# Kernel tuning notes

Measured on AMD Instinct MI355X. Metric: run time of the kernel, lower is better.

Reference implementation:

```python
import jax, jax.numpy as jnp
import numpy as np

N_NODES = 100_000
N_EDGES = 1_600_000
N_GRAPHS = 512
NODE_TYPE_BUCKETS = 256
IDENT_BUCKETS = 50_000
NODE_EMB = 64
IDENT_EMB = 32
IN_DIM = NODE_EMB + IDENT_EMB + 6  # 102
HID = 128
NUM_CATS = 10


def setup_inputs() -> dict:
    key = jax.random.key(0)
    ks = jax.random.split(key, 24)
    p = lambda k, shp: (jax.random.normal(k, shp, dtype=jnp.float32) * 0.05)
    return {
        "node_type_ids": jax.random.randint(ks[0], (N_NODES,), 0, NODE_TYPE_BUCKETS + 2),
        "ident_hash_ids": jax.random.randint(ks[1], (N_NODES,), 0, IDENT_BUCKETS + 2),
        "literal_flags": jax.random.uniform(ks[2], (N_NODES, 5), dtype=jnp.float32),
        "node_depth": jax.random.randint(ks[3], (N_NODES,), 0, 60),
        "edge_index": jax.random.randint(ks[4], (2, N_EDGES), 0, N_NODES),
        "batch_index": jnp.sort(jax.random.randint(ks[5], (N_NODES,), 0, N_GRAPHS)),
        "emb_node": p(ks[6], (NODE_TYPE_BUCKETS + 2, NODE_EMB)),
        "emb_ident": p(ks[7], (IDENT_BUCKETS + 2, IDENT_EMB)),
        "W_self0": p(ks[8], (IN_DIM, HID)), "b_self0": p(ks[9], (HID,)),
        "W_neigh0": p(ks[10], (IN_DIM, HID)), "b_neigh0": p(ks[11], (HID,)),
        "W_self1": p(ks[12], (HID, HID)), "b_self1": p(ks[13], (HID,)),
        "W_neigh1": p(ks[14], (HID, HID)), "b_neigh1": p(ks[15], (HID,)),
        "W_risk": p(ks[16], (HID, 1)), "b_risk": p(ks[17], (1,)),
        "W_cat": p(ks[18], (HID, NUM_CATS)), "b_cat": p(ks[19], (NUM_CATS,)),
    }


def reference(node_type_ids, ident_hash_ids, literal_flags, node_depth,
              edge_index, batch_index, emb_node, emb_ident,
              W_self0, b_self0, W_neigh0, b_neigh0,
              W_self1, b_self1, W_neigh1, b_neigh1,
              W_risk, b_risk, W_cat, b_cat):
    n = node_type_ids.shape[0]
    # node features: [N, 64+32+5+1]
    depth = node_depth.astype(jnp.float32)[:, None]
    depth = depth / jnp.maximum(depth.max(), 1.0)
    x = jnp.concatenate([emb_node[node_type_ids], emb_ident[ident_hash_ids],
                         literal_flags, depth], axis=-1)
    src, dst = edge_index[0], edge_index[1]
    # in-degree, shared across layers (clamped to 1)
    deg = jax.ops.segment_sum(jnp.ones_like(dst, jnp.float32), dst, num_segments=n)
    inv_deg = (1.0 / jnp.maximum(deg, 1.0))[:, None]

    def sage(x, Ws, bs, Wn, bn):
        agg = jax.ops.segment_sum(x[src], dst, num_segments=n)  # gather+scatter-sum
        neigh = agg * inv_deg
        return jax.nn.relu(x @ Ws + bs + neigh @ Wn + bn)

    x = sage(x, W_self0, b_self0, W_neigh0, b_neigh0)
    x = sage(x, W_self1, b_self1, W_neigh1, b_neigh1)

    # global mean pool over graphs
    pooled = jax.ops.segment_sum(x, batch_index, num_segments=N_GRAPHS)
    counts = jax.ops.segment_sum(jnp.ones((n,), jnp.float32), batch_index,
                                 num_segments=N_GRAPHS)
    g = pooled / jnp.maximum(counts, 1.0)[:, None]

    risk_logit = (g @ W_risk + b_risk)[:, 0]
    category_logits = g @ W_cat + b_cat
    return risk_logit, category_logits
```

## Files before the change

kernel.cpp:

```cpp
#include <hip/hip_runtime.h>
#include <cstdint>
#include <cstddef>

#define HIDDIM 128
#define NGRAPH_MAX 512
#define LDSPAD 136
#define NBKT_MAX 512

using short8 = __attribute__((ext_vector_type(8))) short;
using f32x4  = __attribute__((ext_vector_type(4))) float;

__device__ __forceinline__ unsigned short f2bf(float x) {
    union { float f; uint32_t u; } v; v.f = x;
    uint32_t r = v.u + 0x7fffu + ((v.u >> 16) & 1u);
    return (unsigned short)(r >> 16);
}
__device__ __forceinline__ uint32_t pack2(float a, float b) {
    return (uint32_t)f2bf(a) | ((uint32_t)f2bf(b) << 16);
}
__device__ __forceinline__ float bflo(uint32_t u) { return __uint_as_float(u << 16); }
__device__ __forceinline__ float bfhi(uint32_t u) { return __uint_as_float(u & 0xffff0000u); }

__global__ void k_prep(const int* __restrict__ nt, const int* __restrict__ ih,
                       const float* __restrict__ flags, const int* __restrict__ depth,
                       const float* __restrict__ embN, const float* __restrict__ embI,
                       const int* __restrict__ edst, const int* __restrict__ batch,
                       const float* __restrict__ Wn0, const float* __restrict__ Ws0,
                       const float* __restrict__ Wn1, const float* __restrict__ Ws1,
                       int K0, int N, int E, int G,
                       unsigned short* __restrict__ x0, unsigned short* __restrict__ Wt,
                       int* __restrict__ bcount, int* __restrict__ counts,
                       int* __restrict__ maxd,
                       int nbF, int nbC, int nbN) {
    __shared__ int hist[NBKT_MAX];
    __shared__ int red[256];
    int b = blockIdx.x, t = threadIdx.x;
    if (b < nbF) {
        int idx = b * 256 + t;
        int i = idx >> 4;
        int seg = idx & 15;
        if (i >= N) return;
        uint4 o = make_uint4(0u, 0u, 0u, 0u);
        if (seg < 8) {
            const float4* r = (const float4*)(embN + (size_t)nt[i] * 64 + seg * 8);
            float4 v0 = r[0], v1 = r[1];
            o.x = pack2(v0.x, v0.y); o.y = pack2(v0.z, v0.w);
            o.z = pack2(v1.x, v1.y); o.w = pack2(v1.z, v1.w);
        } else if (seg < 12) {
            const float4* r = (const float4*)(embI + (size_t)ih[i] * 32 + (seg - 8) * 8);
            float4 v0 = r[0], v1 = r[1];
            o.x = pack2(v0.x, v0.y); o.y = pack2(v0.z, v0.w);
            o.z = pack2(v1.x, v1.y); o.w = pack2(v1.z, v1.w);
        } else if (seg == 12) {
            const float* fp = flags + (size_t)i * 5;
            o.x = pack2(fp[0], fp[1]);
            o.y = pack2(fp[2], fp[3]);
            o.z = pack2(fp[4], 0.f);
        }
        *(uint4*)(x0 + (size_t)i * HIDDIM + seg * 8) = o;
    } else if (b < nbF + nbC) {
        hist[t] = 0; hist[t + 256] = 0;
        __syncthreads();
        int c0 = (b - nbF) * 4096;
        int ce = min(4096, E - c0);
        for (int i = t; i < ce; i += 256)
            atomicAdd(&hist[edst[c0 + i] >> 8], 1);
        __syncthreads();
        for (int bb = t; bb < NBKT_MAX; bb += 256)
            if (hist[bb]) atomicAdd(&bcount[bb], hist[bb]);
    } else if (b < nbF + nbC + nbN) {
        for (int g = t; g < G; g += 256) hist[g] = 0;
        __syncthreads();
        int i = (b - nbF - nbC) * 256 + t;
        int d = 0;
        if (i < N) {
            atomicAdd(&hist[batch[i]], 1);
            d = depth[i];
        }
        red[t] = d;
        __syncthreads();
        for (int off = 128; off > 0; off >>= 1) {
            if (t < off) red[t] = max(red[t], red[t + off]);
            __syncthreads();
        }
        if (t == 0) atomicMax(maxd, red[0]);
        for (int g = t; g < G; g += 256)
            if (hist[g]) atomicAdd(&counts[g], hist[g]);
    } else {
        int idx = (b - nbF - nbC - nbN) * 256 + t;
        int mat = idx >> 14;
        int rem = idx & 16383;
        int n = rem >> 7, k = rem & 127;
        const float* W = (mat == 0) ? Wn0 : (mat == 1) ? Ws0 : (mat == 2) ? Wn1 : Ws1;
        int K = (mat < 2) ? K0 : HIDDIM;
        Wt[(size_t)mat * HIDDIM * HIDDIM + n * HIDDIM + k] =
            (k < K) ? f2bf(W[(size_t)k * HIDDIM + n]) : (unsigned short)0;
    }
}

__global__ void k_scan2x(const int* __restrict__ bcount, int* __restrict__ boff,
                         int* __restrict__ bcur, int* __restrict__ rowptr,
                         const int* __restrict__ counts, int* __restrict__ gstart,
                         const int* __restrict__ depth, const int* __restrict__ maxd,
                         unsigned short* __restrict__ x0,
                         int nbkt, int N, int E, int G) {
    __shared__ int sd[512];
    int b = blockIdx.x, t = threadIdx.x;
    if (b == 0) {
        int v = (t < nbkt) ? bcount[t] : 0;
        sd[t] = v;
        __syncthreads();
        for (int off = 1; off < 512; off <<= 1) {
            int x = (t >= off) ? sd[t - off] : 0;
            __syncthreads();
            sd[t] += x;
            __syncthreads();
        }
        if (t < nbkt) { boff[t] = sd[t] - v; bcur[t] = sd[t] - v; }
        if (t == 0) { boff[nbkt] = E; rowptr[N] = E; }
    } else if (b == 1) {
        int v = (t < G) ? counts[t] : 0;
        sd[t] = v;
        __syncthreads();
        for (int off = 1; off < 512; off <<= 1) {
            int x = (t >= off) ? sd[t - off] : 0;
            __syncthreads();
            sd[t] += x;
            __syncthreads();
        }
        if (t < G) gstart[t] = sd[t] - v;
        if (t == G - 1) gstart[G] = sd[t];
    } else {
        int i = (b - 2) * 512 + t;
        if (i < N) {
            float md = fmaxf((float)(*maxd), 1.0f);
            x0[(size_t)i * HIDDIM + 101] = f2bf((float)depth[i] / md);
        }
    }
}

__global__ void k_bscatter(const int* __restrict__ src, const int* __restrict__ dst,
                           int* __restrict__ bcur, int2* __restrict__ ebuf, int E, int nbkt) {
    __shared__ int2 stage[4096];
    __shared__ int hist[NBKT_MAX];
    __shared__ int ofs[NBKT_MAX];
    __shared__ int cur[NBKT_MAX];
    __shared__ int gbase[NBKT_MAX];
    __shared__ int scanbuf[256];
    int t = threadIdx.x;
    int c0 = blockIdx.x * 4096;
    int ce = min(4096, E - c0);

    hist[t] = 0; hist[t + 256] = 0;
    __syncthreads();
    for (int i = t; i < ce; i += 256)
        atomicAdd(&hist[dst[c0 + i] >> 8], 1);
    __syncthreads();
    int h2a = hist[2 * t], h2b = hist[2 * t + 1];
    int ps = h2a + h2b;
    scanbuf[t] = ps;
    __syncthreads();
    for (int off = 1; off < 256; off <<= 1) {
        int x = (t >= off) ? scanbuf[t - off] : 0;
        __syncthreads();
        scanbuf[t] += x;
        __syncthreads();
    }
    int ex = scanbuf[t] - ps;
    ofs[2 * t] = ex;           cur[2 * t] = ex;
    ofs[2 * t + 1] = ex + h2a; cur[2 * t + 1] = ex + h2a;
    __syncthreads();
    for (int i = t; i < ce; i += 256) {
        int d = dst[c0 + i];
        int p = atomicAdd(&cur[d >> 8], 1);
        stage[p] = make_int2(src[c0 + i], d);
    }
    __syncthreads();
    for (int b = t; b < nbkt; b += 256) {
        int c = hist[b];
        gbase[b] = c ? atomicAdd(&bcur[b], c) : 0;
    }
    __syncthreads();
    for (int j = t; j < ce; j += 256) {
        int2 p = stage[j];
        int b = p.y >> 8;
        ebuf[gbase[b] + (j - ofs[b])] = p;
    }
}

__global__ void k_build(const int2* __restrict__ ebuf, const int* __restrict__ boff,
                        int* __restrict__ rowptr, float* __restrict__ invd,
                        int* __restrict__ srcs, int N) {
    __shared__ int ldeg[256];
    __shared__ int lofs[256];
    __shared__ int lcur[256];
    int b = blockIdx.x, t = threadIdx.x;
    int n0 = b << 8;
    int s = boff[b], e = boff[b + 1];
    ldeg[t] = 0;
    __syncthreads();
    for (int i = s + t; i < e; i += 256)
        atomicAdd(&ldeg[ebuf[i].y & 255], 1);
    __syncthreads();
    int v = ldeg[t];
    lofs[t] = v;
    __syncthreads();
    for (int off = 1; off < 256; off <<= 1) {
        int x = (t >= off) ? lofs[t - off] : 0;
        __syncthreads();
        lofs[t] += x;
        __syncthreads();
    }
    int excl = lofs[t] - v;
    int node = n0 + t;
    if (node < N) {
        rowptr[node] = s + excl;
        invd[node] = 1.0f / (float)max(v, 1);
    }
    lcur[t] = excl;
    __syncthreads();
    for (int i = s + t; i < e; i += 256) {
        int2 p = ebuf[i];
        int slot = atomicAdd(&lcur[p.y & 255], 1);
        srcs[s + slot] = p.x;
    }
}

__global__ __launch_bounds__(256, 2) void k_gemm2(
    const unsigned short* __restrict__ X,
    const unsigned short* __restrict__ Wtn, const unsigned short* __restrict__ Wts,
    int N, const float* __restrict__ bias_s, const float* __restrict__ bias_n,
    unsigned short* __restrict__ Y, unsigned short* __restrict__ S) {
    __shared__ unsigned short Bn[128 * LDSPAD];
    __shared__ unsigned short Bs[128 * LDSPAD];
    int t = threadIdx.x;
    int rowBase = blockIdx.x << 7;

    #pragma unroll
    for (int it = 0; it < 8; it++) {
        int idx = t + it * 256;
        int n = idx >> 4, seg = idx & 15;
        *(uint4*)&Bn[n * LDSPAD + seg * 8] = *(const uint4*)(Wtn + n * HIDDIM + seg * 8);
        *(uint4*)&Bs[n * LDSPAD + seg * 8] = *(const uint4*)(Wts + n * HIDDIM + seg * 8);
    }

    int lane = t & 63;
    int wv = t >> 6;
    int ml = lane & 15;
    int quad = lane >> 4;
    int m0 = wv * 32;

    const uint4* X4 = (const uint4*)X;
    int gr0 = rowBase + m0 + ml;
    int gr1 = gr0 + 16;
    uint4 af0[4], af1[4];
    #pragma unroll
    for (int kt = 0; kt < 4; kt++) {
        uint4 z = make_uint4(0u, 0u, 0u, 0u);
        af0[kt] = (gr0 < N) ? X4[(size_t)gr0 * 16 + kt * 4 + quad] : z;
        af1[kt] = (gr1 < N) ? X4[(size_t)gr1 * 16 + kt * 4 + quad] : z;
    }
    __syncthreads();

    f32x4 accY[2][8], accS[2][8];
    #pragma unroll
    for (int i = 0; i < 2; i++)
        #pragma unroll
        for (int j = 0; j < 8; j++) {
            accY[i][j] = (f32x4){0.f, 0.f, 0.f, 0.f};
            accS[i][j] = (f32x4){0.f, 0.f, 0.f, 0.f};
        }

    #pragma unroll
    for (int kt = 0; kt < 4; kt++) {
        int ko = kt * 32 + quad * 8;
        short8 a0 = *(short8*)&af0[kt];
        short8 a1 = *(short8*)&af1[kt];
        #pragma unroll
        for (int nt = 0; nt < 8; nt++) {
            short8 bn = *(const short8*)&Bn[(nt * 16 + ml) * LDSPAD + ko];
            accY[0][nt] = __builtin_amdgcn_mfma_f32_16x16x32_bf16(a0, bn, accY[0][nt], 0, 0, 0);
            accY[1][nt] = __builtin_amdgcn_mfma_f32_16x16x32_bf16(a1, bn, accY[1][nt], 0, 0, 0);
            short8 bs = *(const short8*)&Bs[(nt * 16 + ml) * LDSPAD + ko];
            accS[0][nt] = __builtin_amdgcn_mfma_f32_16x16x32_bf16(a0, bs, accS[0][nt], 0, 0, 0);
            accS[1][nt] = __builtin_amdgcn_mfma_f32_16x16x32_bf16(a1, bs, accS[1][nt], 0, 0, 0);
        }
    }

    float bsum[8];
    #pragma unroll
    for (int nt = 0; nt < 8; nt++) {
        int col = nt * 16 + ml;
        bsum[nt] = bias_s[col] + bias_n[col];
    }

    __syncthreads();
    #pragma unroll
    for (int mt = 0; mt < 2; mt++) {
        int lrow0 = m0 + mt * 16 + quad * 4;
        #pragma unroll
        for (int r = 0; r < 4; r++)
            #pragma unroll
            for (int nt = 0; nt < 8; nt++) {
                Bn[(lrow0 + r) * LDSPAD + nt * 16 + ml] = f2bf(accY[mt][nt][r]);
                Bs[(lrow0 + r) * LDSPAD + nt * 16 + ml] = f2bf(accS[mt][nt][r] + bsum[nt]);
            }
    }
    __syncthreads();
    #pragma unroll
    for (int it = 0; it < 8; it++) {
        int idx = t + it * 256;
        int r = idx >> 4, seg = idx & 15;
        int gr = rowBase + r;
        if (gr < N) {
            *(uint4*)(Y + (size_t)gr * HIDDIM + seg * 8) = *(const uint4*)&Bn[r * LDSPAD + seg * 8];
            *(uint4*)(S + (size_t)gr * HIDDIM + seg * 8) = *(const uint4*)&Bs[r * LDSPAD + seg * 8];
        }
    }
}

__global__ void k_aggc(const uint4* __restrict__ y4, const uint4* __restrict__ s4,
                       const int* __restrict__ rp, const int* __restrict__ srcs,
                       const float* __restrict__ invd, uint4* __restrict__ xo, int N) {
    int t = threadIdx.x;
    int lane = t & 63;
    int q = lane >> 4;
    int cl = lane & 15;
    int d = blockIdx.x * 4 + (t >> 6);
    if (d >= N) return;
    int s = rp[d], e = rp[d + 1];
    float a0 = 0.f, a1 = 0.f, a2 = 0.f, a3 = 0.f,
          a4 = 0.f, a5 = 0.f, a6 = 0.f, a7 = 0.f;
#define ACC8(u) { a0 += bflo(u.x); a1 += bfhi(u.x); a2 += bflo(u.y); a3 += bfhi(u.y); \
                  a4 += bflo(u.z); a5 += bfhi(u.z); a6 += bflo(u.w); a7 += bfhi(u.w); }
    for (int base = s; base < e; base += 64) {
        int m = min(64, e - base);
        int idx = (lane < m) ? srcs[base + lane] : 0;
        int j = 0;
        for (; j + 16 <= m; j += 16) {
            int i0 = __shfl(idx, j + q, 64);
            int i1 = __shfl(idx, j + 4 + q, 64);
            int i2 = __shfl(idx, j + 8 + q, 64);
            int i3 = __shfl(idx, j + 12 + q, 64);
            uint4 u0 = y4[(size_t)i0 * 16 + cl];
            uint4 u1 = y4[(size_t)i1 * 16 + cl];
            uint4 u2 = y4[(size_t)i2 * 16 + cl];
            uint4 u3 = y4[(size_t)i3 * 16 + cl];
            ACC8(u0); ACC8(u1); ACC8(u2); ACC8(u3);
        }
        for (; j + 4 <= m; j += 4) {
            int id = __shfl(idx, j + q, 64);
            uint4 u = y4[(size_t)id * 16 + cl];
            ACC8(u);
        }
        if (j < m) {
            int id = __shfl(idx, min(j + q, m - 1), 64);
            if (q < m - j) {
                uint4 u = y4[(size_t)id * 16 + cl];
                ACC8(u);
            }
        }
    }
#undef ACC8
    a0 += __shfl_down(a0, 32, 64); a1 += __shfl_down(a1, 32, 64);
    a2 += __shfl_down(a2, 32, 64); a3 += __shfl_down(a3, 32, 64);
    a4 += __shfl_down(a4, 32, 64); a5 += __shfl_down(a5, 32, 64);
    a6 += __shfl_down(a6, 32, 64); a7 += __shfl_down(a7, 32, 64);
    a0 += __shfl_down(a0, 16, 64); a1 += __shfl_down(a1, 16, 64);
    a2 += __shfl_down(a2, 16, 64); a3 += __shfl_down(a3, 16, 64);
    a4 += __shfl_down(a4, 16, 64); a5 += __shfl_down(a5, 16, 64);
    a6 += __shfl_down(a6, 16, 64); a7 += __shfl_down(a7, 16, 64);
    if (q == 0) {
        float iv = invd[d];
        uint4 su = s4[(size_t)d * 16 + cl];
        uint4 o;
        o.x = pack2(fmaxf(bflo(su.x) + a0 * iv, 0.f), fmaxf(bfhi(su.x) + a1 * iv, 0.f));
        o.y = pack2(fmaxf(bflo(su.y) + a2 * iv, 0.f), fmaxf(bfhi(su.y) + a3 * iv, 0.f));
        o.z = pack2(fmaxf(bflo(su.z) + a4 * iv, 0.f), fmaxf(bfhi(su.z) + a5 * iv, 0.f));
        o.w = pack2(fmaxf(bflo(su.w) + a6 * iv, 0.f), fmaxf(bfhi(su.w) + a7 * iv, 0.f));
        xo[(size_t)d * 16 + cl] = o;
    }
}

__global__ void k_poolhead(const uint32_t* __restrict__ x, const int* __restrict__ gstart,
                           const int* __restrict__ counts,
                           const float* __restrict__ Wr, const float* __restrict__ br,
                           const float* __restrict__ Wc, const float* __restrict__ bc,
                           float* __restrict__ out, int G) {
    __shared__ float red[3][128];
    __shared__ float rowf[128];
    int gr = blockIdx.x, t = threadIdx.x;
    int wv = t >> 6, lane = t & 63;
    int half = lane >> 5, cl = lane & 31;
    int s = gstart[gr], e = gstart[gr + 1];
    const uint2* x2 = (const uint2*)x;
    float a0 = 0.f, a1 = 0.f, a2 = 0.f, a3 = 0.f;
    for (int r0 = s + wv * 2 + half; r0 < e; r0 += 32) {
        uint2 u0 = x2[(size_t)r0 * 32 + cl];
        int r1 = r0 + 8, r2 = r0 + 16, r3 = r0 + 24;
        uint2 u1 = make_uint2(0u, 0u), u2 = make_uint2(0u, 0u), u3 = make_uint2(0u, 0u);
        if (r1 < e) u1 = x2[(size_t)r1 * 32 + cl];
        if (r2 < e) u2 = x2[(size_t)r2 * 32 + cl];
        if (r3 < e) u3 = x2[(size_t)r3 * 32 + cl];
        a0 += bflo(u0.x); a1 += bfhi(u0.x); a2 += bflo(u0.y); a3 += bfhi(u0.y);
        a0 += bflo(u1.x); a1 += bfhi(u1.x); a2 += bflo(u1.y); a3 += bfhi(u1.y);
        a0 += bflo(u2.x); a1 += bfhi(u2.x); a2 += bflo(u2.y); a3 += bfhi(u2.y);
        a0 += bflo(u3.x); a1 += bfhi(u3.x); a2 += bflo(u3.y); a3 += bfhi(u3.y);
    }
    a0 += __shfl_down(a0, 32, 64);
    a1 += __shfl_down(a1, 32, 64);
    a2 += __shfl_down(a2, 32, 64);
    a3 += __shfl_down(a3, 32, 64);
    if (half == 0 && wv > 0) {
        red[wv - 1][cl * 4 + 0] = a0;
        red[wv - 1][cl * 4 + 1] = a1;
        red[wv - 1][cl * 4 + 2] = a2;
        red[wv - 1][cl * 4 + 3] = a3;
    }
    __syncthreads();
    if (wv == 0 && half == 0) {
        a0 += red[0][cl * 4 + 0] + red[1][cl * 4 + 0] + red[2][cl * 4 + 0];
        a1 += red[0][cl * 4 + 1] + red[1][cl * 4 + 1] + red[2][cl * 4 + 1];
        a2 += red[0][cl * 4 + 2] + red[1][cl * 4 + 2] + red[2][cl * 4 + 2];
        a3 += red[0][cl * 4 + 3] + red[1][cl * 4 + 3] + red[2][cl * 4 + 3];
        float inv = 1.0f / fmaxf((float)counts[gr], 1.0f);
        rowf[cl * 4 + 0] = a0 * inv;
        rowf[cl * 4 + 1] = a1 * inv;
        rowf[cl * 4 + 2] = a2 * inv;
        rowf[cl * 4 + 3] = a3 * inv;
    }
    __syncthreads();
    if (t == 0) {
        float s2 = 0.f;
        for (int k = 0; k < 128; k++) s2 += rowf[k] * Wr[k];
        out[gr] = s2 + br[0];
    } else if (t <= 10) {
        int j = t - 1;
        float s2 = 0.f;
        for (int k = 0; k < 128; k++) s2 += rowf[k] * Wc[k * 10 + j];
        out[G + gr * 10 + j] = s2 + bc[j];
    }
}

extern "C" void kernel_launch(void* const* d_in, const int* in_sizes, int n_in,
                              void* d_out, int out_size, void* d_ws, size_t ws_size,
                              hipStream_t stream) {
    const int*   nt    = (const int*)d_in[0];
    const int*   ih    = (const int*)d_in[1];
    const float* flags = (const float*)d_in[2];
    const int*   depth = (const int*)d_in[3];
    const int*   eidx  = (const int*)d_in[4];
    const int*   batch = (const int*)d_in[5];
    const float* embN  = (const float*)d_in[6];
    const float* embI  = (const float*)d_in[7];
    const float* Ws0   = (const float*)d_in[8];
    const float* bs0   = (const float*)d_in[9];
    const float* Wn0   = (const float*)d_in[10];
    const float* bn0   = (const float*)d_in[11];
    const float* Ws1   = (const float*)d_in[12];
    const float* bs1   = (const float*)d_in[13];
    const float* Wn1   = (const float*)d_in[14];
    const float* bn1   = (const float*)d_in[15];
    const float* Wr    = (const float*)d_in[16];
    const float* br    = (const float*)d_in[17];
    const float* Wc    = (const float*)d_in[18];
    const float* bc    = (const float*)d_in[19];
    float* out = (float*)d_out;

    const int N  = in_sizes[0];
    const int E  = in_sizes[4] / 2;
    const int K0 = in_sizes[8] / HIDDIM;
    const int G  = out_size / 11;
    const int* esrc = eidx;
    const int* edst = eidx + E;
    const int NBKT = (N + 255) >> 8;

    char* w = (char*)d_ws;
    const size_t NH = (size_t)N * HIDDIM * sizeof(unsigned short);
    unsigned short* bufA = (unsigned short*)(w);
    unsigned short* bufY = (unsigned short*)(w + NH);
    unsigned short* bufS = (unsigned short*)(w + 2 * NH);
    unsigned short* bufX1= (unsigned short*)(w + 3 * NH);
    char* p = w + 4 * NH;
    unsigned short* Wt = (unsigned short*)p; p += (size_t)4 * HIDDIM * HIDDIM * 2;
    int2* ebuf  = (int2*)p;          p += (size_t)E * 8;
    int* srcs   = (int*)p;           p += (size_t)E * 4;
    int* rowptr = (int*)p;           p += (size_t)(N + 1) * 4;
    float* invd = (float*)p;         p += (size_t)N * 4;
    int* gstart = (int*)p;           p += (size_t)(G + 1) * 4;
    int* boff   = (int*)p;           p += (size_t)(NBKT_MAX + 1) * 4;
    int* bcur   = (int*)p;           p += (size_t)NBKT_MAX * 4;
    int* bcount = (int*)p;           p += (size_t)NBKT_MAX * 4;
    int* counts = (int*)p;           p += (size_t)G * 4;
    int* maxd   = (int*)p;           p += 4;
    const size_t zero_bytes = (size_t)(NBKT_MAX + G + 1) * 4;
    (void)n_in; (void)ws_size;

    const int nbC = (E + 4095) / 4096;
    const int nbN = (N + 255) / 256;
    const int nbF = ((size_t)N * 16 + 255) / 256;
    const int nbG2 = (N + 127) / 128;
    const int nbA = (N + 3) / 4;
    const int nbD = (N + 511) / 512;

    hipMemsetAsync(bcount, 0, zero_bytes, stream);

    k_prep<<<nbF + nbC + nbN + 256, 256, 0, stream>>>(
        nt, ih, flags, depth, embN, embI, edst, batch,
        Wn0, Ws0, Wn1, Ws1, K0, N, E, G,
        bufA, Wt, bcount, counts, maxd, nbF, nbC, nbN);

    k_scan2x<<<2 + nbD, 512, 0, stream>>>(bcount, boff, bcur, rowptr,
                                          counts, gstart, depth, maxd, bufA,
                                          NBKT, N, E, G);

    k_bscatter<<<nbC, 256, 0, stream>>>(esrc, edst, bcur, ebuf, E, NBKT);
    k_build<<<NBKT, 256, 0, stream>>>(ebuf, boff, rowptr, invd, srcs, N);

    const unsigned short* Wt_n0 = Wt;
    const unsigned short* Wt_s0 = Wt + 1 * HIDDIM * HIDDIM;
    const unsigned short* Wt_n1 = Wt + 2 * HIDDIM * HIDDIM;
    const unsigned short* Wt_s1 = Wt + 3 * HIDDIM * HIDDIM;

    k_gemm2<<<nbG2, 256, 0, stream>>>(bufA, Wt_n0, Wt_s0, N, bs0, bn0, bufY, bufS);
    k_aggc<<<nbA, 256, 0, stream>>>((const uint4*)bufY, (const uint4*)bufS,
                                    rowptr, srcs, invd, (uint4*)bufX1, N);

    k_gemm2<<<nbG2, 256, 0, stream>>>(bufX1, Wt_n1, Wt_s1, N, bs1, bn1, bufY, bufS);
    k_aggc<<<nbA, 256, 0, stream>>>((const uint4*)bufY, (const uint4*)bufS,
                                    rowptr, srcs, invd, (uint4*)bufA, N);

    k_poolhead<<<G, 256, 0, stream>>>((const uint32_t*)bufA, gstart, counts,
                                      Wr, br, Wc, bc, out, G);
}
```

Before: 361.3 us.

## Store node features in column-sliced layout so aggregation gathers per 16-column slice

Node feature buffers become 8 column slices of 16 bf16 values, each slice laid out contiguously across all nodes. The prep, GEMM, aggregation and pooling kernels all index this layout, and aggregation launches 8 blocks per node group so each block gathers one 32-byte slice per neighbour. The aim is a smaller working set per slice (about 3.2 MB per slice instead of 25.6 MB per feature array), so random neighbour gathers hit in cache more often. The cost is 8x more aggregation blocks, each rereading the CSR row pointers and source indices, and narrower 4-byte loads per lane.

```diff
diff --git a/kernel.cpp b/kernel.cpp
--- a/kernel.cpp
+++ b/kernel.cpp
@@ -6,6 +6,7 @@
 #define NGRAPH_MAX 512
 #define LDSPAD 136
 #define NBKT_MAX 512
+
 
 using short8 = __attribute__((ext_vector_type(8))) short;
 using f32x4  = __attribute__((ext_vector_type(4))) float;
@@ -28,7 +29,7 @@
                        const float* __restrict__ Wn0, const float* __restrict__ Ws0,
                        const float* __restrict__ Wn1, const float* __restrict__ Ws1,
                        int K0, int N, int E, int G,
-                       unsigned short* __restrict__ x0, unsigned short* __restrict__ Wt,
+                       uint4* __restrict__ x0s, unsigned short* __restrict__ Wt,
                        int* __restrict__ bcount, int* __restrict__ counts,
                        int* __restrict__ maxd,
                        int nbF, int nbC, int nbN) {
@@ -57,7 +58,7 @@
             o.y = pack2(fp[2], fp[3]);
             o.z = pack2(fp[4], 0.f);
         }
-        *(uint4*)(x0 + (size_t)i * HIDDIM + seg * 8) = o;
+        x0s[(size_t)(seg >> 1) * (N * 2) + (size_t)i * 2 + (seg & 1)] = o;
     } else if (b < nbF + nbC) {
         hist[t] = 0; hist[t + 256] = 0;
         __syncthreads();
@@ -102,7 +103,7 @@
                          int* __restrict__ bcur, int* __restrict__ rowptr,
                          const int* __restrict__ counts, int* __restrict__ gstart,
                          const int* __restrict__ depth, const int* __restrict__ maxd,
-                         unsigned short* __restrict__ x0,
+                         unsigned short* __restrict__ x0s,
                          int nbkt, int N, int E, int G) {
     __shared__ int sd[512];
     int b = blockIdx.x, t = threadIdx.x;
@@ -134,7 +135,7 @@
         int i = (b - 2) * 512 + t;
         if (i < N) {
             float md = fmaxf((float)(*maxd), 1.0f);
-            x0[(size_t)i * HIDDIM + 101] = f2bf((float)depth[i] / md);
+            x0s[(size_t)6 * N * 16 + (size_t)i * 16 + 5] = f2bf((float)depth[i] / md);
         }
     }
 }
@@ -227,14 +228,15 @@
 }
 
 __global__ __launch_bounds__(256, 2) void k_gemm2(
-    const unsigned short* __restrict__ X,
+    const uint4* __restrict__ Xs,
     const unsigned short* __restrict__ Wtn, const unsigned short* __restrict__ Wts,
     int N, const float* __restrict__ bias_s, const float* __restrict__ bias_n,
-    unsigned short* __restrict__ Y, unsigned short* __restrict__ S) {
+    uint4* __restrict__ Ys, uint4* __restrict__ Ss) {
     __shared__ unsigned short Bn[128 * LDSPAD];
     __shared__ unsigned short Bs[128 * LDSPAD];
     int t = threadIdx.x;
     int rowBase = blockIdx.x << 7;
+    const size_t N2 = (size_t)N * 2;
 
     #pragma unroll
     for (int it = 0; it < 8; it++) {
@@ -250,15 +252,15 @@
     int quad = lane >> 4;
     int m0 = wv * 32;
 
-    const uint4* X4 = (const uint4*)X;
     int gr0 = rowBase + m0 + ml;
     int gr1 = gr0 + 16;
     uint4 af0[4], af1[4];
     #pragma unroll
     for (int kt = 0; kt < 4; kt++) {
         uint4 z = make_uint4(0u, 0u, 0u, 0u);
-        af0[kt] = (gr0 < N) ? X4[(size_t)gr0 * 16 + kt * 4 + quad] : z;
-        af1[kt] = (gr1 < N) ? X4[(size_t)gr1 * 16 + kt * 4 + quad] : z;
+        size_t sb = (size_t)(2 * kt + (quad >> 1)) * N2 + (quad & 1);
+        af0[kt] = (gr0 < N) ? Xs[sb + (size_t)gr0 * 2] : z;
+        af1[kt] = (gr1 < N) ? Xs[sb + (size_t)gr1 * 2] : z;
     }
     __syncthreads();
 
@@ -313,121 +315,111 @@
         int r = idx >> 4, seg = idx & 15;
         int gr = rowBase + r;
         if (gr < N) {
-            *(uint4*)(Y + (size_t)gr * HIDDIM + seg * 8) = *(const uint4*)&Bn[r * LDSPAD + seg * 8];
-            *(uint4*)(S + (size_t)gr * HIDDIM + seg * 8) = *(const uint4*)&Bs[r * LDSPAD + seg * 8];
-        }
-    }
-}
-
-__global__ void k_aggc(const uint4* __restrict__ y4, const uint4* __restrict__ s4,
+            size_t o = (size_t)(seg >> 1) * N2 + (size_t)gr * 2 + (seg & 1);
+            Ys[o] = *(const uint4*)&Bn[r * LDSPAD + seg * 8];
+            Ss[o] = *(const uint4*)&Bs[r * LDSPAD + seg * 8];
+        }
+    }
+}
+
+__global__ void k_aggc(const uint32_t* __restrict__ ys, const uint32_t* __restrict__ ss,
                        const int* __restrict__ rp, const int* __restrict__ srcs,
-                       const float* __restrict__ invd, uint4* __restrict__ xo, int N) {
+                       const float* __restrict__ invd, uint32_t* __restrict__ xos, int N) {
     int t = threadIdx.x;
     int lane = t & 63;
-    int q = lane >> 4;
-    int cl = lane & 15;
-    int d = blockIdx.x * 4 + (t >> 6);
+    int q = lane >> 3;
+    int cl = lane & 7;
+    int slice = blockIdx.x & 7;
+    int d = (blockIdx.x >> 3) * 4 + (t >> 6);
     if (d >= N) return;
+    const uint32_t* yb = ys + (size_t)slice * N * 8;
     int s = rp[d], e = rp[d + 1];
-    float a0 = 0.f, a1 = 0.f, a2 = 0.f, a3 = 0.f,
-          a4 = 0.f, a5 = 0.f, a6 = 0.f, a7 = 0.f;
-#define ACC8(u) { a0 += bflo(u.x); a1 += bfhi(u.x); a2 += bflo(u.y); a3 += bfhi(u.y); \
-                  a4 += bflo(u.z); a5 += bfhi(u.z); a6 += bflo(u.w); a7 += bfhi(u.w); }
+    float a0 = 0.f, a1 = 0.f;
     for (int base = s; base < e; base += 64) {
         int m = min(64, e - base);
         int idx = (lane < m) ? srcs[base + lane] : 0;
         int j = 0;
-        for (; j + 16 <= m; j += 16) {
+        for (; j + 32 <= m; j += 32) {
             int i0 = __shfl(idx, j + q, 64);
-            int i1 = __shfl(idx, j + 4 + q, 64);
-            int i2 = __shfl(idx, j + 8 + q, 64);
-            int i3 = __shfl(idx, j + 12 + q, 64);
-            uint4 u0 = y4[(size_t)i0 * 16 + cl];
-            uint4 u1 = y4[(size_t)i1 * 16 + cl];
-            uint4 u2 = y4[(size_t)i2 * 16 + cl];
-            uint4 u3 = y4[(size_t)i3 * 16 + cl];
-            ACC8(u0); ACC8(u1); ACC8(u2); ACC8(u3);
-        }
-        for (; j + 4 <= m; j += 4) {
+            int i1 = __shfl(idx, j + 8 + q, 64);
+            int i2 = __shfl(idx, j + 16 + q, 64);
+            int i3 = __shfl(idx, j + 24 + q, 64);
+            uint32_t u0 = yb[(size_t)i0 * 8 + cl];
+            uint32_t u1 = yb[(size_t)i1 * 8 + cl];
+            uint32_t u2 = yb[(size_t)i2 * 8 + cl];
+            uint32_t u3 = yb[(size_t)i3 * 8 + cl];
+            a0 += bflo(u0); a1 += bfhi(u0);
+            a0 += bflo(u1); a1 += bfhi(u1);
+            a0 += bflo(u2); a1 += bfhi(u2);
+            a0 += bflo(u3); a1 += bfhi(u3);
+        }
+        for (; j + 8 <= m; j += 8) {
             int id = __shfl(idx, j + q, 64);
-            uint4 u = y4[(size_t)id * 16 + cl];
-            ACC8(u);
+            uint32_t u = yb[(size_t)id * 8 + cl];
+            a0 += bflo(u); a1 += bfhi(u);
         }
         if (j < m) {
             int id = __shfl(idx, min(j + q, m - 1), 64);
             if (q < m - j) {
-                uint4 u = y4[(size_t)id * 16 + cl];
-                ACC8(u);
+                uint32_t u = yb[(size_t)id * 8 + cl];
+                a0 += bflo(u); a1 += bfhi(u);
             }
         }
     }
-#undef ACC8
     a0 += __shfl_down(a0, 32, 64); a1 += __shfl_down(a1, 32, 64);
-    a2 += __shfl_down(a2, 32, 64); a3 += __shfl_down(a3, 32, 64);
-    a4 += __shfl_down(a4, 32, 64); a5 += __shfl_down(a5, 32, 64);
-    a6 += __shfl_down(a6, 32, 64); a7 += __shfl_down(a7, 32, 64);
     a0 += __shfl_down(a0, 16, 64); a1 += __shfl_down(a1, 16, 64);
-    a2 += __shfl_down(a2, 16, 64); a3 += __shfl_down(a3, 16, 64);
-    a4 += __shfl_down(a4, 16, 64); a5 += __shfl_down(a5, 16, 64);
-    a6 += __shfl_down(a6, 16, 64); a7 += __shfl_down(a7, 16, 64);
+    a0 += __shfl_down(a0, 8, 64);  a1 += __shfl_down(a1, 8, 64);
     if (q == 0) {
         float iv = invd[d];
-        uint4 su = s4[(size_t)d * 16 + cl];
-        uint4 o;
-        o.x = pack2(fmaxf(bflo(su.x) + a0 * iv, 0.f), fmaxf(bfhi(su.x) + a1 * iv, 0.f));
-        o.y = pack2(fmaxf(bflo(su.y) + a2 * iv, 0.f), fmaxf(bfhi(su.y) + a3 * iv, 0.f));
-        o.z = pack2(fmaxf(bflo(su.z) + a4 * iv, 0.f), fmaxf(bfhi(su.z) + a5 * iv, 0.f));
-        o.w = pack2(fmaxf(bflo(su.w) + a6 * iv, 0.f), fmaxf(bfhi(su.w) + a7 * iv, 0.f));
-        xo[(size_t)d * 16 + cl] = o;
-    }
-}
-
-__global__ void k_poolhead(const uint32_t* __restrict__ x, const int* __restrict__ gstart,
+        size_t o = (size_t)slice * N * 8 + (size_t)d * 8 + cl;
+        uint32_t su = ss[o];
+        xos[o] = pack2(fmaxf(bflo(su) + a0 * iv, 0.f),
+                       fmaxf(bfhi(su) + a1 * iv, 0.f));
+    }
+}
+
+__global__ void k_poolhead(const uint4* __restrict__ xs, const int* __restrict__ gstart,
                            const int* __restrict__ counts,
                            const float* __restrict__ Wr, const float* __restrict__ br,
                            const float* __restrict__ Wc, const float* __restrict__ bc,
-                           float* __restrict__ out, int G) {
+                           float* __restrict__ out, int N, int G) {
     __shared__ float red[3][128];
     __shared__ float rowf[128];
     int gr = blockIdx.x, t = threadIdx.x;
     int wv = t >> 6, lane = t & 63;
-    int half = lane >> 5, cl = lane & 31;
+    int q = lane >> 4;
+    int cl = lane & 15;
     int s = gstart[gr], e = gstart[gr + 1];
-    const uint2* x2 = (const uint2*)x;
-    float a0 = 0.f, a1 = 0.f, a2 = 0.f, a3 = 0.f;
-    for (int r0 = s + wv * 2 + half; r0 < e; r0 += 32) {
-        uint2 u0 = x2[(size_t)r0 * 32 + cl];
-        int r1 = r0 + 8, r2 = r0 + 16, r3 = r0 + 24;
-        uint2 u1 = make_uint2(0u, 0u), u2 = make_uint2(0u, 0u), u3 = make_uint2(0u, 0u);
-        if (r1 < e) u1 = x2[(size_t)r1 * 32 + cl];
-        if (r2 < e) u2 = x2[(size_t)r2 * 32 + cl];
-        if (r3 < e) u3 = x2[(size_t)r3 * 32 + cl];
-        a0 += bflo(u0.x); a1 += bfhi(u0.x); a2 += bflo(u0.y); a3 += bfhi(u0.y);
-        a0 += bflo(u1.x); a1 += bfhi(u1.x); a2 += bflo(u1.y); a3 += bfhi(u1.y);
-        a0 += bflo(u2.x); a1 += bfhi(u2.x); a2 += bflo(u2.y); a3 += bfhi(u2.y);
-        a0 += bflo(u3.x); a1 += bfhi(u3.x); a2 += bflo(u3.y); a3 += bfhi(u3.y);
-    }
-    a0 += __shfl_down(a0, 32, 64);
-    a1 += __shfl_down(a1, 32, 64);
-    a2 += __shfl_down(a2, 32, 64);
-    a3 += __shfl_down(a3, 32, 64);
-    if (half == 0 && wv > 0) {
-        red[wv - 1][cl * 4 + 0] = a0;
-        red[wv - 1][cl * 4 + 1] = a1;
-        red[wv - 1][cl * 4 + 2] = a2;
-        red[wv - 1][cl * 4 + 3] = a3;
-    }
-    __syncthreads();
-    if (wv == 0 && half == 0) {
-        a0 += red[0][cl * 4 + 0] + red[1][cl * 4 + 0] + red[2][cl * 4 + 0];
-        a1 += red[0][cl * 4 + 1] + red[1][cl * 4 + 1] + red[2][cl * 4 + 1];
-        a2 += red[0][cl * 4 + 2] + red[1][cl * 4 + 2] + red[2][cl * 4 + 2];
-        a3 += red[0][cl * 4 + 3] + red[1][cl * 4 + 3] + red[2][cl * 4 + 3];
+    const size_t N2 = (size_t)N * 2;
+    size_t sb = (size_t)(cl >> 1) * N2 + (cl & 1);
+    float a[8] = {0.f, 0.f, 0.f, 0.f, 0.f, 0.f, 0.f, 0.f};
+    for (int r0 = s + wv * 4 + q; r0 < e; r0 += 32) {
+        uint4 u0 = xs[sb + (size_t)r0 * 2];
+        uint4 u1 = make_uint4(0u, 0u, 0u, 0u);
+        int r1 = r0 + 16;
+        if (r1 < e) u1 = xs[sb + (size_t)r1 * 2];
+        a[0] += bflo(u0.x) + bflo(u1.x); a[1] += bfhi(u0.x) + bfhi(u1.x);
+        a[2] += bflo(u0.y) + bflo(u1.y); a[3] += bfhi(u0.y) + bfhi(u1.y);
+        a[4] += bflo(u0.z) + bflo(u1.z); a[5] += bfhi(u0.z) + bfhi(u1.z);
+        a[6] += bflo(u0.w) + bflo(u1.w); a[7] += bfhi(u0.w) + bfhi(u1.w);
+    }
+    #pragma unroll
+    for (int i = 0; i < 8; i++) {
+        a[i] += __shfl_down(a[i], 32, 64);
+        a[i] += __shfl_down(a[i], 16, 64);
+    }
+    if (q == 0 && wv > 0) {
+        #pragma unroll
+        for (int i = 0; i < 8; i++) red[wv - 1][cl * 8 + i] = a[i];
+    }
+    __syncthreads();
+    if (wv == 0 && q == 0) {
         float inv = 1.0f / fmaxf((float)counts[gr], 1.0f);
-        rowf[cl * 4 + 0] = a0 * inv;
-        rowf[cl * 4 + 1] = a1 * inv;
-        rowf[cl * 4 + 2] = a2 * inv;
-        rowf[cl * 4 + 3] = a3 * inv;
+        #pragma unroll
+        for (int i = 0; i < 8; i++) {
+            float v = a[i] + red[0][cl * 8 + i] + red[1][cl * 8 + i] + red[2][cl * 8 + i];
+            rowf[cl * 8 + i] = v * inv;
+        }
     }
     __syncthreads();
     if (t == 0) {
@@ -500,7 +492,7 @@
     const int nbN = (N + 255) / 256;
     const int nbF = ((size_t)N * 16 + 255) / 256;
     const int nbG2 = (N + 127) / 128;
-    const int nbA = (N + 3) / 4;
+    const int nbA8 = ((N + 3) / 4) * 8;
     const int nbD = (N + 511) / 512;
 
     hipMemsetAsync(bcount, 0, zero_bytes, stream);
@@ -508,7 +500,7 @@
     k_prep<<<nbF + nbC + nbN + 256, 256, 0, stream>>>(
         nt, ih, flags, depth, embN, embI, edst, batch,
         Wn0, Ws0, Wn1, Ws1, K0, N, E, G,
-        bufA, Wt, bcount, counts, maxd, nbF, nbC, nbN);
+        (uint4*)bufA, Wt, bcount, counts, maxd, nbF, nbC, nbN);
 
     k_scan2x<<<2 + nbD, 512, 0, stream>>>(bcount, boff, bcur, rowptr,
                                           counts, gstart, depth, maxd, bufA,
@@ -522,14 +514,16 @@
     const unsigned short* Wt_n1 = Wt + 2 * HIDDIM * HIDDIM;
     const unsigned short* Wt_s1 = Wt + 3 * HIDDIM * HIDDIM;
 
-    k_gemm2<<<nbG2, 256, 0, stream>>>(bufA, Wt_n0, Wt_s0, N, bs0, bn0, bufY, bufS);
-    k_aggc<<<nbA, 256, 0, stream>>>((const uint4*)bufY, (const uint4*)bufS,
-                                    rowptr, srcs, invd, (uint4*)bufX1, N);
-
-    k_gemm2<<<nbG2, 256, 0, stream>>>(bufX1, Wt_n1, Wt_s1, N, bs1, bn1, bufY, bufS);
-    k_aggc<<<nbA, 256, 0, stream>>>((const uint4*)bufY, (const uint4*)bufS,
-                                    rowptr, srcs, invd, (uint4*)bufA, N);
-
-    k_poolhead<<<G, 256, 0, stream>>>((const uint32_t*)bufA, gstart, counts,
-                                      Wr, br, Wc, bc, out, G);
-}
+    k_gemm2<<<nbG2, 256, 0, stream>>>((const uint4*)bufA, Wt_n0, Wt_s0, N, bs0, bn0,
+                                      (uint4*)bufY, (uint4*)bufS);
+    k_aggc<<<nbA8, 256, 0, stream>>>((const uint32_t*)bufY, (const uint32_t*)bufS,
+                                     rowptr, srcs, invd, (uint32_t*)bufX1, N);
+
+    k_gemm2<<<nbG2, 256, 0, stream>>>((const uint4*)bufX1, Wt_n1, Wt_s1, N, bs1, bn1,
+                                      (uint4*)bufY, (uint4*)bufS);
+    k_aggc<<<nbA8, 256, 0, stream>>>((const uint32_t*)bufY, (const uint32_t*)bufS,
+                                     rowptr, srcs, invd, (uint32_t*)bufA, N);
+
+    k_poolhead<<<G, 256, 0, stream>>>((const uint4*)bufA, gstart, counts,
+                                      Wr, br, Wc, bc, out, N, G);
+}
```

After: 667.7 us. 1.85x slower.

## Aggregate raw features before the transform and pack edge buffer entries into 32 bits

Applied to the files above, without the earlier changes.

Each SAGE layer now first mean-aggregates the input features over neighbors. A new fused GEMM then computes X·Ws + AX·Wn + bias with ReLU and writes a single output. This replaces projecting to separate Y and S buffers and combining them in the aggregation kernel, which removes one full N×128 intermediate write and read per layer. The edge staging buffer now packs the source index and the low 8 bits of the destination into one 32-bit word, halving its traffic; this assumes node ids fit in 24 bits. The scatter's final copy is now a per-bucket serial loop per thread, which may coalesce less well, and a leftover dead loop remains.

```diff
diff --git a/kernel.cpp b/kernel.cpp
--- a/kernel.cpp
+++ b/kernel.cpp
@@ -6,6 +6,7 @@
 #define NGRAPH_MAX 512
 #define LDSPAD 136
 #define NBKT_MAX 512
+
 
 using short8 = __attribute__((ext_vector_type(8))) short;
 using f32x4  = __attribute__((ext_vector_type(4))) float;
@@ -140,8 +141,8 @@
 }
 
 __global__ void k_bscatter(const int* __restrict__ src, const int* __restrict__ dst,
-                           int* __restrict__ bcur, int2* __restrict__ ebuf, int E, int nbkt) {
-    __shared__ int2 stage[4096];
+                           int* __restrict__ bcur, uint32_t* __restrict__ ebuf, int E, int nbkt) {
+    __shared__ uint32_t stage[4096];
     __shared__ int hist[NBKT_MAX];
     __shared__ int ofs[NBKT_MAX];
     __shared__ int cur[NBKT_MAX];
@@ -173,7 +174,7 @@
     for (int i = t; i < ce; i += 256) {
         int d = dst[c0 + i];
         int p = atomicAdd(&cur[d >> 8], 1);
-        stage[p] = make_int2(src[c0 + i], d);
+        stage[p] = (uint32_t)src[c0 + i] | ((uint32_t)(d & 255) << 24);
     }
     __syncthreads();
     for (int b = t; b < nbkt; b += 256) {
@@ -182,13 +183,22 @@
     }
     __syncthreads();
     for (int j = t; j < ce; j += 256) {
-        int2 p = stage[j];
-        int b = p.y >> 8;
-        ebuf[gbase[b] + (j - ofs[b])] = p;
-    }
-}
-
-__global__ void k_build(const int2* __restrict__ ebuf, const int* __restrict__ boff,
+        uint32_t p = stage[j];
+        (void)p;
+        break;
+    }
+    __syncthreads();
+    for (int b = t; b < nbkt; b += 256) {
+        int cnt = hist[b];
+        if (!cnt) continue;
+        int lo = ofs[b];
+        int gb = gbase[b];
+        for (int k = 0; k < cnt; k++)
+            ebuf[gb + k] = stage[lo + k];
+    }
+}
+
+__global__ void k_build(const uint32_t* __restrict__ ebuf, const int* __restrict__ boff,
                         int* __restrict__ rowptr, float* __restrict__ invd,
                         int* __restrict__ srcs, int N) {
     __shared__ int ldeg[256];
@@ -200,7 +210,7 @@
     ldeg[t] = 0;
     __syncthreads();
     for (int i = s + t; i < e; i += 256)
-        atomicAdd(&ldeg[ebuf[i].y & 255], 1);
+        atomicAdd(&ldeg[ebuf[i] >> 24], 1);
     __syncthreads();
     int v = ldeg[t];
     lofs[t] = v;
@@ -220,108 +230,15 @@
     lcur[t] = excl;
     __syncthreads();
     for (int i = s + t; i < e; i += 256) {
-        int2 p = ebuf[i];
-        int slot = atomicAdd(&lcur[p.y & 255], 1);
-        srcs[s + slot] = p.x;
-    }
-}
-
-__global__ __launch_bounds__(256, 2) void k_gemm2(
-    const unsigned short* __restrict__ X,
-    const unsigned short* __restrict__ Wtn, const unsigned short* __restrict__ Wts,
-    int N, const float* __restrict__ bias_s, const float* __restrict__ bias_n,
-    unsigned short* __restrict__ Y, unsigned short* __restrict__ S) {
-    __shared__ unsigned short Bn[128 * LDSPAD];
-    __shared__ unsigned short Bs[128 * LDSPAD];
-    int t = threadIdx.x;
-    int rowBase = blockIdx.x << 7;
-
-    #pragma unroll
-    for (int it = 0; it < 8; it++) {
-        int idx = t + it * 256;
-        int n = idx >> 4, seg = idx & 15;
-        *(uint4*)&Bn[n * LDSPAD + seg * 8] = *(const uint4*)(Wtn + n * HIDDIM + seg * 8);
-        *(uint4*)&Bs[n * LDSPAD + seg * 8] = *(const uint4*)(Wts + n * HIDDIM + seg * 8);
-    }
-
-    int lane = t & 63;
-    int wv = t >> 6;
-    int ml = lane & 15;
-    int quad = lane >> 4;
-    int m0 = wv * 32;
-
-    const uint4* X4 = (const uint4*)X;
-    int gr0 = rowBase + m0 + ml;
-    int gr1 = gr0 + 16;
-    uint4 af0[4], af1[4];
-    #pragma unroll
-    for (int kt = 0; kt < 4; kt++) {
-        uint4 z = make_uint4(0u, 0u, 0u, 0u);
-        af0[kt] = (gr0 < N) ? X4[(size_t)gr0 * 16 + kt * 4 + quad] : z;
-        af1[kt] = (gr1 < N) ? X4[(size_t)gr1 * 16 + kt * 4 + quad] : z;
-    }
-    __syncthreads();
-
-    f32x4 accY[2][8], accS[2][8];
-    #pragma unroll
-    for (int i = 0; i < 2; i++)
-        #pragma unroll
-        for (int j = 0; j < 8; j++) {
-            accY[i][j] = (f32x4){0.f, 0.f, 0.f, 0.f};
-            accS[i][j] = (f32x4){0.f, 0.f, 0.f, 0.f};
-        }
-
-    #pragma unroll
-    for (int kt = 0; kt < 4; kt++) {
-        int ko = kt * 32 + quad * 8;
-        short8 a0 = *(short8*)&af0[kt];
-        short8 a1 = *(short8*)&af1[kt];
-        #pragma unroll
-        for (int nt = 0; nt < 8; nt++) {
-            short8 bn = *(const short8*)&Bn[(nt * 16 + ml) * LDSPAD + ko];
-            accY[0][nt] = __builtin_amdgcn_mfma_f32_16x16x32_bf16(a0, bn, accY[0][nt], 0, 0, 0);
-            accY[1][nt] = __builtin_amdgcn_mfma_f32_16x16x32_bf16(a1, bn, accY[1][nt], 0, 0, 0);
-            short8 bs = *(const short8*)&Bs[(nt * 16 + ml) * LDSPAD + ko];
-            accS[0][nt] = __builtin_amdgcn_mfma_f32_16x16x32_bf16(a0, bs, accS[0][nt], 0, 0, 0);
-            accS[1][nt] = __builtin_amdgcn_mfma_f32_16x16x32_bf16(a1, bs, accS[1][nt], 0, 0, 0);
-        }
-    }
-
-    float bsum[8];
-    #pragma unroll
-    for (int nt = 0; nt < 8; nt++) {
-        int col = nt * 16 + ml;
-        bsum[nt] = bias_s[col] + bias_n[col];
-    }
-
-    __syncthreads();
-    #pragma unroll
-    for (int mt = 0; mt < 2; mt++) {
-        int lrow0 = m0 + mt * 16 + quad * 4;
-        #pragma unroll
-        for (int r = 0; r < 4; r++)
-            #pragma unroll
-            for (int nt = 0; nt < 8; nt++) {
-                Bn[(lrow0 + r) * LDSPAD + nt * 16 + ml] = f2bf(accY[mt][nt][r]);
-                Bs[(lrow0 + r) * LDSPAD + nt * 16 + ml] = f2bf(accS[mt][nt][r] + bsum[nt]);
-            }
-    }
-    __syncthreads();
-    #pragma unroll
-    for (int it = 0; it < 8; it++) {
-        int idx = t + it * 256;
-        int r = idx >> 4, seg = idx & 15;
-        int gr = rowBase + r;
-        if (gr < N) {
-            *(uint4*)(Y + (size_t)gr * HIDDIM + seg * 8) = *(const uint4*)&Bn[r * LDSPAD + seg * 8];
-            *(uint4*)(S + (size_t)gr * HIDDIM + seg * 8) = *(const uint4*)&Bs[r * LDSPAD + seg * 8];
-        }
-    }
-}
-
-__global__ void k_aggc(const uint4* __restrict__ y4, const uint4* __restrict__ s4,
-                       const int* __restrict__ rp, const int* __restrict__ srcs,
-                       const float* __restrict__ invd, uint4* __restrict__ xo, int N) {
+        uint32_t p = ebuf[i];
+        int slot = atomicAdd(&lcur[p >> 24], 1);
+        srcs[s + slot] = (int)(p & 0x00FFFFFFu);
+    }
+}
+
+__global__ void k_aggc(const uint4* __restrict__ x4, const int* __restrict__ rp,
+                       const int* __restrict__ srcs, const float* __restrict__ invd,
+                       uint4* __restrict__ axo, int N) {
     int t = threadIdx.x;
     int lane = t & 63;
     int q = lane >> 4;
@@ -342,21 +259,21 @@
             int i1 = __shfl(idx, j + 4 + q, 64);
             int i2 = __shfl(idx, j + 8 + q, 64);
             int i3 = __shfl(idx, j + 12 + q, 64);
-            uint4 u0 = y4[(size_t)i0 * 16 + cl];
-            uint4 u1 = y4[(size_t)i1 * 16 + cl];
-            uint4 u2 = y4[(size_t)i2 * 16 + cl];
-            uint4 u3 = y4[(size_t)i3 * 16 + cl];
+            uint4 u0 = x4[(size_t)i0 * 16 + cl];
+            uint4 u1 = x4[(size_t)i1 * 16 + cl];
+            uint4 u2 = x4[(size_t)i2 * 16 + cl];
+            uint4 u3 = x4[(size_t)i3 * 16 + cl];
             ACC8(u0); ACC8(u1); ACC8(u2); ACC8(u3);
         }
         for (; j + 4 <= m; j += 4) {
             int id = __shfl(idx, j + q, 64);
-            uint4 u = y4[(size_t)id * 16 + cl];
+            uint4 u = x4[(size_t)id * 16 + cl];
             ACC8(u);
         }
         if (j < m) {
             int id = __shfl(idx, min(j + q, m - 1), 64);
             if (q < m - j) {
-                uint4 u = y4[(size_t)id * 16 + cl];
+                uint4 u = x4[(size_t)id * 16 + cl];
                 ACC8(u);
             }
         }
@@ -372,13 +289,106 @@
     a6 += __shfl_down(a6, 16, 64); a7 += __shfl_down(a7, 16, 64);
     if (q == 0) {
         float iv = invd[d];
-        uint4 su = s4[(size_t)d * 16 + cl];
         uint4 o;
-        o.x = pack2(fmaxf(bflo(su.x) + a0 * iv, 0.f), fmaxf(bfhi(su.x) + a1 * iv, 0.f));
-        o.y = pack2(fmaxf(bflo(su.y) + a2 * iv, 0.f), fmaxf(bfhi(su.y) + a3 * iv, 0.f));
-        o.z = pack2(fmaxf(bflo(su.z) + a4 * iv, 0.f), fmaxf(bfhi(su.z) + a5 * iv, 0.f));
-        o.w = pack2(fmaxf(bflo(su.w) + a6 * iv, 0.f), fmaxf(bfhi(su.w) + a7 * iv, 0.f));
-        xo[(size_t)d * 16 + cl] = o;
+        o.x = pack2(a0 * iv, a1 * iv);
+        o.y = pack2(a2 * iv, a3 * iv);
+        o.z = pack2(a4 * iv, a5 * iv);
+        o.w = pack2(a6 * iv, a7 * iv);
+        axo[(size_t)d * 16 + cl] = o;
+    }
+}
+
+__global__ __launch_bounds__(256, 2) void k_gemm3(
+    const unsigned short* __restrict__ X, const unsigned short* __restrict__ AX,
+    const unsigned short* __restrict__ Wts, const unsigned short* __restrict__ Wtn,
+    int N, const float* __restrict__ bias_s, const float* __restrict__ bias_n,
+    unsigned short* __restrict__ Xo) {
+    __shared__ unsigned short Bs[128 * LDSPAD];
+    __shared__ unsigned short Bn[128 * LDSPAD];
+    int t = threadIdx.x;
+    int rowBase = blockIdx.x << 7;
+
+    #pragma unroll
+    for (int it = 0; it < 8; it++) {
+        int idx = t + it * 256;
+        int n = idx >> 4, seg = idx & 15;
+        *(uint4*)&Bs[n * LDSPAD + seg * 8] = *(const uint4*)(Wts + n * HIDDIM + seg * 8);
+        *(uint4*)&Bn[n * LDSPAD + seg * 8] = *(const uint4*)(Wtn + n * HIDDIM + seg * 8);
+    }
+
+    int lane = t & 63;
+    int wv = t >> 6;
+    int ml = lane & 15;
+    int quad = lane >> 4;
+    int m0 = wv * 32;
+
+    const uint4* X4 = (const uint4*)X;
+    const uint4* A4 = (const uint4*)AX;
+    int gr0 = rowBase + m0 + ml;
+    int gr1 = gr0 + 16;
+    uint4 fx0[4], fx1[4], fa0[4], fa1[4];
+    #pragma unroll
+    for (int kt = 0; kt < 4; kt++) {
+        uint4 z = make_uint4(0u, 0u, 0u, 0u);
+        size_t o0 = (size_t)gr0 * 16 + kt * 4 + quad;
+        size_t o1 = (size_t)gr1 * 16 + kt * 4 + quad;
+        fx0[kt] = (gr0 < N) ? X4[o0] : z;
+        fx1[kt] = (gr1 < N) ? X4[o1] : z;
+        fa0[kt] = (gr0 < N) ? A4[o0] : z;
+        fa1[kt] = (gr1 < N) ? A4[o1] : z;
+    }
+    __syncthreads();
+
+    f32x4 acc[2][8];
+    #pragma unroll
+    for (int i = 0; i < 2; i++)
+        #pragma unroll
+        for (int j = 0; j < 8; j++) acc[i][j] = (f32x4){0.f, 0.f, 0.f, 0.f};
+
+    #pragma unroll
+    for (int kt = 0; kt < 4; kt++) {
+        int ko = kt * 32 + quad * 8;
+        short8 x0f = *(short8*)&fx0[kt];
+        short8 x1f = *(short8*)&fx1[kt];
+        short8 a0f = *(short8*)&fa0[kt];
+        short8 a1f = *(short8*)&fa1[kt];
+        #pragma unroll
+        for (int nt = 0; nt < 8; nt++) {
+            short8 bs = *(const short8*)&Bs[(nt * 16 + ml) * LDSPAD + ko];
+            short8 bn = *(const short8*)&Bn[(nt * 16 + ml) * LDSPAD + ko];
+            acc[0][nt] = __builtin_amdgcn_mfma_f32_16x16x32_bf16(x0f, bs, acc[0][nt], 0, 0, 0);
+            acc[1][nt] = __builtin_amdgcn_mfma_f32_16x16x32_bf16(x1f, bs, acc[1][nt], 0, 0, 0);
+            acc[0][nt] = __builtin_amdgcn_mfma_f32_16x16x32_bf16(a0f, bn, acc[0][nt], 0, 0, 0);
+            acc[1][nt] = __builtin_amdgcn_mfma_f32_16x16x32_bf16(a1f, bn, acc[1][nt], 0, 0, 0);
+        }
+    }
+
+    float bsum[8];
+    #pragma unroll
+    for (int nt = 0; nt < 8; nt++) {
+        int col = nt * 16 + ml;
+        bsum[nt] = bias_s[col] + bias_n[col];
+    }
+
+    __syncthreads();
+    #pragma unroll
+    for (int mt = 0; mt < 2; mt++) {
+        int lrow0 = m0 + mt * 16 + quad * 4;
+        #pragma unroll
+        for (int r = 0; r < 4; r++)
+            #pragma unroll
+            for (int nt = 0; nt < 8; nt++)
+                Bs[(lrow0 + r) * LDSPAD + nt * 16 + ml] =
+                    f2bf(fmaxf(acc[mt][nt][r] + bsum[nt], 0.f));
+    }
+    __syncthreads();
+    #pragma unroll
+    for (int it = 0; it < 8; it++) {
+        int idx = t + it * 256;
+        int r = idx >> 4, seg = idx & 15;
+        int gr = rowBase + r;
+        if (gr < N)
+            *(uint4*)(Xo + (size_t)gr * HIDDIM + seg * 8) = *(const uint4*)&Bs[r * LDSPAD + seg * 8];
     }
 }
 
@@ -477,13 +487,12 @@
 
     char* w = (char*)d_ws;
     const size_t NH = (size_t)N * HIDDIM * sizeof(unsigned short);
-    unsigned short* bufA = (unsigned short*)(w);
-    unsigned short* bufY = (unsigned short*)(w + NH);
-    unsigned short* bufS = (unsigned short*)(w + 2 * NH);
-    unsigned short* bufX1= (unsigned short*)(w + 3 * NH);
-    char* p = w + 4 * NH;
+    unsigned short* bufA  = (unsigned short*)(w);
+    unsigned short* bufB  = (unsigned short*)(w + NH);
+    unsigned short* bufAX = (unsigned short*)(w + 2 * NH);
+    char* p = w + 3 * NH;
     unsigned short* Wt = (unsigned short*)p; p += (size_t)4 * HIDDIM * HIDDIM * 2;
-    int2* ebuf  = (int2*)p;          p += (size_t)E * 8;
+    uint32_t* ebuf = (uint32_t*)p;   p += (size_t)E * 4;
     int* srcs   = (int*)p;           p += (size_t)E * 4;
     int* rowptr = (int*)p;           p += (size_t)(N + 1) * 4;
     float* invd = (float*)p;         p += (size_t)N * 4;
@@ -522,13 +531,13 @@
     const unsigned short* Wt_n1 = Wt + 2 * HIDDIM * HIDDIM;
     const unsigned short* Wt_s1 = Wt + 3 * HIDDIM * HIDDIM;
 
-    k_gemm2<<<nbG2, 256, 0, stream>>>(bufA, Wt_n0, Wt_s0, N, bs0, bn0, bufY, bufS);
-    k_aggc<<<nbA, 256, 0, stream>>>((const uint4*)bufY, (const uint4*)bufS,
-                                    rowptr, srcs, invd, (uint4*)bufX1, N);
-
-    k_gemm2<<<nbG2, 256, 0, stream>>>(bufX1, Wt_n1, Wt_s1, N, bs1, bn1, bufY, bufS);
-    k_aggc<<<nbA, 256, 0, stream>>>((const uint4*)bufY, (const uint4*)bufS,
-                                    rowptr, srcs, invd, (uint4*)bufA, N);
+    k_aggc<<<nbA, 256, 0, stream>>>((const uint4*)bufA, rowptr, srcs, invd,
+                                    (uint4*)bufAX, N);
+    k_gemm3<<<nbG2, 256, 0, stream>>>(bufA, bufAX, Wt_s0, Wt_n0, N, bs0, bn0, bufB);
+
+    k_aggc<<<nbA, 256, 0, stream>>>((const uint4*)bufB, rowptr, srcs, invd,
+                                    (uint4*)bufAX, N);
+    k_gemm3<<<nbG2, 256, 0, stream>>>(bufB, bufAX, Wt_s1, Wt_n1, N, bs1, bn1, bufA);
 
     k_poolhead<<<G, 256, 0, stream>>>((const uint32_t*)bufA, gstart, counts,
                                       Wr, br, Wc, bc, out, G);
```

Result: faster. 342.5 us (-5.2%).
